# Performance work log

Hardware: AMD Instinct MI355X
Metric: run time of the kernel (lower is better)

The kernel has to match this reference:

```python
import jax, jax.numpy as jnp
import numpy as np

B, N, E = 8, 10000, 320000
HIST, PRED = 24, 12
IN_DIM, GNN_OUT, HID = 17, 13, 64


def setup_inputs() -> dict:
    key = jax.random.key(0)
    ks = jax.random.split(key, 16)
    rn = lambda k, s, sc=0.1: jax.random.normal(k, s, jnp.float32) * sc
    return {
        "t2m_hist": jax.random.normal(ks[0], (B, HIST, N, 1), jnp.float32),
        "feature": jax.random.normal(ks[1], (B, HIST + PRED, N, IN_DIM - 1), jnp.float32),
        "edge_index": jax.random.randint(ks[2], (2, E), 0, N),
        "edge_attr": jax.random.normal(ks[3], (E, 1), jnp.float32),
        "edge_w1": rn(ks[4], (2 * IN_DIM + 1, 32)),
        "edge_b1": rn(ks[5], (32,)),
        "edge_w2": rn(ks[6], (32, 30)),
        "edge_b2": rn(ks[7], (30,)),
        "node_w": rn(ks[8], (30, GNN_OUT)),
        "node_b": rn(ks[9], (GNN_OUT,)),
        "gru_wih": rn(ks[10], (3 * HID, IN_DIM + GNN_OUT)),
        "gru_whh": rn(ks[11], (3 * HID, HID)),
        "gru_bih": rn(ks[12], (3 * HID,)),
        "gru_bhh": rn(ks[13], (3 * HID,)),
        "fc_out_w": rn(ks[14], (HID, 1)),
        "fc_out_b": rn(ks[15], (1,)),
    }


def reference(t2m_hist, feature, edge_index, edge_attr,
              edge_w1, edge_b1, edge_w2, edge_b2, node_w, node_b,
              gru_wih, gru_whh, gru_bih, gru_bhh, fc_out_w, fc_out_b):
    src, tgt = edge_index[0], edge_index[1]
    # edge_attr normalized with unbiased std (torch default)
    ea_norm = (edge_attr - edge_attr.mean(0)) / edge_attr.std(0, ddof=1)  # [E,1]

    def graph_gnn(x):  # x: [B,N,IN_DIM]
        ns = x[:, src]                                  # [B,E,IN_DIM] gather
        nt = x[:, tgt]                                  # [B,E,IN_DIM] gather
        ea = jnp.broadcast_to(ea_norm[None], (B, E, 1))
        h = jnp.concatenate([ns, nt, ea], axis=-1)      # [B,E,2*IN_DIM+1]
        h = jax.nn.sigmoid(h @ edge_w1 + edge_b1)
        h = jax.nn.sigmoid(h @ edge_w2 + edge_b2)       # [B,E,30]
        agg = jnp.zeros((B, N, 30), h.dtype)
        agg = agg.at[:, tgt].add(h)                     # scatter_add to targets
        agg = agg.at[:, src].add(-h)                    # scatter_add(-) to sources
        return jax.nn.sigmoid(agg @ node_w + node_b)    # [B,N,GNN_OUT]

    def gru(xin, h):  # xin: [M,30], h: [M,HID]  (PyTorch GRUCell math)
        gi = xin @ gru_wih.T + gru_bih
        gh = h @ gru_whh.T + gru_bhh
        i_r, i_z, i_n = jnp.split(gi, 3, axis=-1)
        h_r, h_z, h_n = jnp.split(gh, 3, axis=-1)
        r = jax.nn.sigmoid(i_r + h_r)
        z = jax.nn.sigmoid(i_z + h_z)
        n = jnp.tanh(i_n + r * h_n)
        return (1.0 - z) * n + z * h

    feat_future = jnp.moveaxis(feature[:, HIST:HIST + PRED], 1, 0)  # [PRED,B,N,16]
    h0 = jnp.zeros((B * N, HID), jnp.float32)
    xn0 = t2m_hist[:, -1]  # [B,N,1]

    def step(carry, feat_t):
        hn, xn = carry
        x = jnp.concatenate([xn, feat_t], axis=-1)      # [B,N,IN_DIM]
        g = graph_gnn(x)                                # [B,N,GNN_OUT]
        xin = jnp.concatenate([g, x], axis=-1).reshape(B * N, IN_DIM + GNN_OUT)
        hn = gru(xin, hn)
        xn = hn.reshape(B, N, HID) @ fc_out_w + fc_out_b  # [B,N,1]
        return (hn, xn), xn

    _, preds = jax.lax.scan(step, (h0, xn0), feat_future)  # [PRED,B,N,1]
    return jnp.moveaxis(preds, 0, 1)                        # [B,PRED,N,1]
```

## Files before the change

### kernel.cpp

```cpp
#include <hip/hip_runtime.h>
#include <hip/hip_fp16.h>
#include <hip/hip_bf16.h>

#define Bb 8
#define Nn 10000
#define Ee 320000
#define HIST 24
#define PRED 12
#define BN (Bb * Nn)

__device__ __forceinline__ float sigm(float x) { return 1.0f / (1.0f + __expf(-x)); }
__device__ __forceinline__ float tanh_fast(float x) { return 1.0f - 2.0f / (__expf(2.0f * x) + 1.0f); }

__device__ __forceinline__ void load16f(const float* p, float* o) {
  const float4* q = reinterpret_cast<const float4*>(p);
  float4 a = q[0], b = q[1], c = q[2], d = q[3];
  o[0] = a.x; o[1] = a.y; o[2]  = a.z; o[3]  = a.w;
  o[4] = b.x; o[5] = b.y; o[6]  = b.z; o[7]  = b.w;
  o[8] = c.x; o[9] = c.y; o[10] = c.z; o[11] = c.w;
  o[12] = d.x; o[13] = d.y; o[14] = d.z; o[15] = d.w;
}

__device__ __forceinline__ void edge_mlp(const float* __restrict__ in,
                                         const float* __restrict__ W,
                                         float* __restrict__ h2) {
  const float* w1 = W;
  const float* b1 = W + 1120;
  const float* w2 = W + 1152;
  const float* b2 = W + 2112;
  float h1[32];
#pragma unroll
  for (int j = 0; j < 32; j++) h1[j] = b1[j];
#pragma unroll
  for (int k = 0; k < 35; k++) {
    float v = in[k];
#pragma unroll
    for (int j = 0; j < 32; j++) h1[j] = fmaf(v, w1[k * 32 + j], h1[j]);
  }
#pragma unroll
  for (int j = 0; j < 32; j++) h1[j] = sigm(h1[j]);
#pragma unroll
  for (int j = 0; j < 30; j++) h2[j] = b2[j];
#pragma unroll
  for (int k = 0; k < 32; k++) {
    float v = h1[k];
#pragma unroll
    for (int j = 0; j < 30; j++) h2[j] = fmaf(v, w2[k * 30 + j], h2[j]);
  }
#pragma unroll
  for (int j = 0; j < 30; j++) h2[j] = sigm(h2[j]);
}

__device__ __forceinline__ void gru_out(const float* __restrict__ agg,
                                        const float* __restrict__ W,
                                        const float* __restrict__ featp,
                                        float xn_old,
                                        float* __restrict__ xn_new_slot,
                                        float* __restrict__ hp,
                                        float* __restrict__ out_slot) {
  const float* nw  = W + 2142;
  const float* nb  = W + 2532;
  const float* wih = W + 2545;
  const float* whh = W + 8305;
  const float* bih = W + 20593;
  const float* bhh = W + 20785;
  const float* fw  = W + 20977;
  const float* fcb = W + 21041;
  float xin[30];
#pragma unroll
  for (int j = 0; j < 13; j++) {
    float a = nb[j];
#pragma unroll
    for (int k = 0; k < 30; k++) a = fmaf(agg[k], nw[k * 13 + j], a);
    xin[j] = sigm(a);
  }
  xin[13] = xn_old;
  load16f(featp, xin + 14);
  float h[64];
#pragma unroll
  for (int j = 0; j < 64; j++) h[j] = hp[j];
  float xnew = fcb[0];
  for (int j = 0; j < 64; j++) {
    float ir = bih[j], iz = bih[64 + j], inn = bih[128 + j];
    const float* wr = wih + j * 30;
    const float* wz = wih + (64 + j) * 30;
    const float* wn = wih + (128 + j) * 30;
#pragma unroll
    for (int k = 0; k < 30; k++) {
      ir  = fmaf(xin[k], wr[k], ir);
      iz  = fmaf(xin[k], wz[k], iz);
      inn = fmaf(xin[k], wn[k], inn);
    }
    float hr = bhh[j], hz = bhh[64 + j], hn_ = bhh[128 + j];
    const float* vr = whh + j * 64;
    const float* vz = whh + (64 + j) * 64;
    const float* vn = whh + (128 + j) * 64;
#pragma unroll
    for (int k = 0; k < 64; k++) {
      hr  = fmaf(h[k], vr[k], hr);
      hz  = fmaf(h[k], vz[k], hz);
      hn_ = fmaf(h[k], vn[k], hn_);
    }
    float rg = sigm(ir + hr);
    float zg = sigm(iz + hz);
    float ng = tanh_fast(inn + rg * hn_);
    float hnew = (1.f - zg) * ng + zg * h[j];
    hp[j] = hnew;
    xnew = fmaf(hnew, fw[j], xnew);
  }
  *xn_new_slot = xnew;
  *out_slot = xnew;
}


__global__ void k_stats(const float* __restrict__ ea, float* __restrict__ stats) {
  __shared__ float s1[256], s2[256];
  int tid = threadIdx.x;
  int i = blockIdx.x * 256 + tid;
  float v = 0.f;
  if (i < Ee) v = ea[i];
  s1[tid] = v;
  s2[tid] = v * v;
  __syncthreads();
  for (int o = 128; o > 0; o >>= 1) {
    if (tid < o) { s1[tid] += s1[tid + o]; s2[tid] += s2[tid + o]; }
    __syncthreads();
  }
  if (tid == 0) { atomicAdd(&stats[0], s1[0]); atomicAdd(&stats[1], s2[0]); }
}

__global__ void k_finalize_stats(float* stats) {
  float sum = stats[0], sumsq = stats[1];
  float mean = sum / (float)Ee;
  float var = (sumsq - sum * mean) / (float)(Ee - 1);
  stats[2] = mean;
  stats[3] = rsqrtf(var);
}

__global__ void k_hist(const int* __restrict__ eidx, int* __restrict__ deg_t, int* __restrict__ deg_s) {
  int e = blockIdx.x * 256 + threadIdx.x;
  if (e >= Ee) return;
  atomicAdd(&deg_s[eidx[e]], 1);
  atomicAdd(&deg_t[eidx[Ee + e]], 1);
}

__global__ void k_scan(const int* __restrict__ deg_t, int* __restrict__ off_t,
                       const int* __restrict__ deg_s, int* __restrict__ off_s) {
  const int* deg = (blockIdx.x == 0) ? deg_t : deg_s;
  int* off = (blockIdx.x == 0) ? off_t : off_s;
  __shared__ int s[1024];
  __shared__ int carry;
  int tid = threadIdx.x;
  if (tid == 0) carry = 0;
  __syncthreads();
  for (int base = 0; base < Nn; base += 1024) {
    int v = (base + tid < Nn) ? deg[base + tid] : 0;
    s[tid] = v;
    int val = v;
    __syncthreads();
    for (int o = 1; o < 1024; o <<= 1) {
      int tv = (tid >= o) ? s[tid - o] : 0;
      __syncthreads();
      val += tv;
      s[tid] = val;
      __syncthreads();
    }
    if (base + tid < Nn) off[base + tid] = carry + (val - v);
    __syncthreads();
    if (tid == 1023) carry += val;
    __syncthreads();
  }
  if (tid == 0) off[Nn] = carry;
}

__global__ void k_fill(const int* __restrict__ eidx,
                       const int* __restrict__ off_t, const int* __restrict__ off_s,
                       int* __restrict__ cur_t, int* __restrict__ cur_s,
                       int* __restrict__ list_t, int* __restrict__ list_s) {
  int e = blockIdx.x * 256 + threadIdx.x;
  if (e >= Ee) return;
  int s = eidx[e], t = eidx[Ee + e];
  int ps = off_s[s] + atomicAdd(&cur_s[s], 1);
  list_s[ps] = e;
  int pt = off_t[t] + atomicAdd(&cur_t[t], 1);
  list_t[pt] = e;
}

__global__ void k_convert(const float* w1, const float* b1, const float* w2, const float* b2,
                          const float* nw, const float* nb, const float* wih, const float* whh,
                          const float* bih, const float* bhh, const float* fw, const float* fb,
                          float* __restrict__ dst) {
  int i = blockIdx.x * 256 + threadIdx.x;
  const int c1 = 1120, c2 = 1152, c3 = 2112, c4 = 2142, c5 = 2532, c6 = 2545,
            c7 = 8305, c8 = 20593, c9 = 20785, c10 = 20977, c11 = 21041, c12 = 21042;
  if (i >= c12) return;
  const float* p;
  int base;
  if (i < c1)       { p = w1;  base = 0;  }
  else if (i < c2)  { p = b1;  base = c1; }
  else if (i < c3)  { p = w2;  base = c2; }
  else if (i < c4)  { p = b2;  base = c3; }
  else if (i < c5)  { p = nw;  base = c4; }
  else if (i < c6)  { p = nb;  base = c5; }
  else if (i < c7)  { p = wih; base = c6; }
  else if (i < c8)  { p = whh; base = c7; }
  else if (i < c9)  { p = bih; base = c8; }
  else if (i < c10) { p = bhh; base = c9; }
  else if (i < c11) { p = fw;  base = c10; }
  else              { p = fb;  base = c11; }
  dst[i] = p[i - base];
}

__global__ void k_xn0(const float* __restrict__ t2m, float* __restrict__ xn) {
  int i = blockIdx.x * 256 + threadIdx.x;
  if (i >= BN) return;
  int b = i / Nn, n = i % Nn;
  xn[i] = t2m[((size_t)b * HIST + (HIST - 1)) * Nn + n];
}


__global__ __launch_bounds__(256) void k_pre_edge(
    const float* __restrict__ feat, const float* __restrict__ xn,
    const float* __restrict__ W, float* __restrict__ as_, float* __restrict__ at_, int t) {
  int idx = blockIdx.x * 256 + threadIdx.x;
  if (idx >= BN) return;
  int b = idx / Nn, n = idx % Nn;
  const float* w1 = W;
  const float* b1 = W + 1120;
  float f[16];
  const float* fbp = feat + ((size_t)(b * (HIST + PRED) + HIST + t)) * Nn * 16 + (size_t)n * 16;
  load16f(fbp, f);
  float x = xn[idx];
  float as[32], at[32];
#pragma unroll
  for (int j = 0; j < 32; j++) {
    as[j] = fmaf(x, w1[j], b1[j]);
    at[j] = x * w1[17 * 32 + j];
  }
#pragma unroll
  for (int k = 0; k < 16; k++) {
    float v = f[k];
#pragma unroll
    for (int j = 0; j < 32; j++) {
      as[j] = fmaf(v, w1[(1 + k) * 32 + j], as[j]);
      at[j] = fmaf(v, w1[(18 + k) * 32 + j], at[j]);
    }
  }
  float4* ap = (float4*)(as_ + (size_t)idx * 32);
  float4* bp = (float4*)(at_ + (size_t)idx * 32);
#pragma unroll
  for (int q = 0; q < 8; q++) {
    ap[q] = make_float4(as[4 * q], as[4 * q + 1], as[4 * q + 2], as[4 * q + 3]);
    bp[q] = make_float4(at[4 * q], at[4 * q + 1], at[4 * q + 2], at[4 * q + 3]);
  }
}

__global__ __launch_bounds__(256) void k_edge2(
    const int* __restrict__ eidx, const float* __restrict__ ea,
    const float* __restrict__ as_, const float* __restrict__ at_,
    const float* __restrict__ W, const float* __restrict__ stats,
    __half* __restrict__ h2out) {
  int e = blockIdx.x * 256 + threadIdx.x;
  int b = blockIdx.y;
  if (e >= Ee) return;
  float mean = stats[2], istd = stats[3];
  int s = eidx[e], tg = eidx[Ee + e];
  float ean = (ea[e] - mean) * istd;
  const float* w1e = W + 34 * 32;
  const float* w2 = W + 1152;
  const float* b2 = W + 2112;
  const float4* ap = (const float4*)(as_ + ((size_t)(b * Nn + s)) * 32);
  const float4* bp = (const float4*)(at_ + ((size_t)(b * Nn + tg)) * 32);
  float h1[32];
#pragma unroll
  for (int q = 0; q < 8; q++) {
    float4 av = ap[q], bv = bp[q];
    h1[4 * q]     = av.x + bv.x;
    h1[4 * q + 1] = av.y + bv.y;
    h1[4 * q + 2] = av.z + bv.z;
    h1[4 * q + 3] = av.w + bv.w;
  }
#pragma unroll
  for (int j = 0; j < 32; j++) h1[j] = sigm(fmaf(ean, w1e[j], h1[j]));
  float h2[30];
#pragma unroll
  for (int j = 0; j < 30; j++) h2[j] = b2[j];
#pragma unroll
  for (int k = 0; k < 32; k++) {
    float v = h1[k];
#pragma unroll
    for (int j = 0; j < 30; j++) h2[j] = fmaf(v, w2[k * 30 + j], h2[j]);
  }
  __half2* o = (__half2*)(h2out + ((size_t)b * Ee + e) * 30);
#pragma unroll
  for (int i = 0; i < 15; i++) o[i] = __floats2half2_rn(sigm(h2[2 * i]), sigm(h2[2 * i + 1]));
}

__global__ __launch_bounds__(256) void k_edge(
    const int* __restrict__ eidx, const float* __restrict__ ea,
    const float* __restrict__ feat, const float* __restrict__ xn,
    const float* __restrict__ W, const float* __restrict__ stats,
    __half* __restrict__ h2out, int t) {
  int e = blockIdx.x * 256 + threadIdx.x;
  int b = blockIdx.y;
  if (e >= Ee) return;
  float mean = stats[2], istd = stats[3];
  int s = eidx[e], tg = eidx[Ee + e];
  float in[35];
  in[0]  = xn[b * Nn + s];
  in[17] = xn[b * Nn + tg];
  in[34] = (ea[e] - mean) * istd;
  const float* fb = feat + ((size_t)(b * (HIST + PRED) + HIST + t)) * Nn * 16;
  load16f(fb + (size_t)s * 16, in + 1);
  load16f(fb + (size_t)tg * 16, in + 18);
  float h2[30];
  edge_mlp(in, W, h2);
  __half2* o = (__half2*)(h2out + ((size_t)b * Ee + e) * 30);
#pragma unroll
  for (int i = 0; i < 15; i++) o[i] = __floats2half2_rn(h2[2 * i], h2[2 * i + 1]);
}

__global__ __launch_bounds__(256) void k_gather(
    const int* __restrict__ off_t, const int* __restrict__ list_t,
    const int* __restrict__ off_s, const int* __restrict__ list_s,
    const __half* __restrict__ h2, float* __restrict__ agg) {
  int tid = threadIdx.x;
  int c = tid & 31;
  int idx = blockIdx.x * 8 + (tid >> 5);
  if (idx >= BN || c >= 30) return;
  int b = idx / Nn, n = idx % Nn;
  const __half* base = h2 + (size_t)b * Ee * 30;
  float a = 0.f;
  int p0 = off_t[n], p1 = off_t[n + 1];
  int p = p0;
  for (; p + 4 <= p1; p += 4) {
    int e0 = list_t[p], e1 = list_t[p + 1], e2 = list_t[p + 2], e3 = list_t[p + 3];
    float v0 = __half2float(base[(size_t)e0 * 30 + c]);
    float v1 = __half2float(base[(size_t)e1 * 30 + c]);
    float v2 = __half2float(base[(size_t)e2 * 30 + c]);
    float v3 = __half2float(base[(size_t)e3 * 30 + c]);
    a += (v0 + v1) + (v2 + v3);
  }
  for (; p < p1; p++) a += __half2float(base[(size_t)list_t[p] * 30 + c]);
  p0 = off_s[n]; p1 = off_s[n + 1];
  p = p0;
  for (; p + 4 <= p1; p += 4) {
    int e0 = list_s[p], e1 = list_s[p + 1], e2 = list_s[p + 2], e3 = list_s[p + 3];
    float v0 = __half2float(base[(size_t)e0 * 30 + c]);
    float v1 = __half2float(base[(size_t)e1 * 30 + c]);
    float v2 = __half2float(base[(size_t)e2 * 30 + c]);
    float v3 = __half2float(base[(size_t)e3 * 30 + c]);
    a -= (v0 + v1) + (v2 + v3);
  }
  for (; p < p1; p++) a -= __half2float(base[(size_t)list_s[p] * 30 + c]);
  agg[(size_t)idx * 30 + c] = a;
}

#define HS_STRIDE 68

__global__ __launch_bounds__(256, 4) void k_gru4(
    const float* __restrict__ agg_all, const float* __restrict__ W,
    const float* __restrict__ feat, const float* __restrict__ xn_cur,
    float* __restrict__ xn_nxt, float* __restrict__ hbuf,
    float* __restrict__ out, int t) {
  __shared__ float hs[64 * HS_STRIDE];
  __shared__ float sx[4][64];

  const int tid = threadIdx.x;
  const int lane = tid & 63;
  const int wave = (int)__builtin_amdgcn_readfirstlane(tid >> 6);
  const int node = blockIdx.x * 64 + lane;
  const int b = node / Nn, n = node % Nn;

  const float* nw  = W + 2142;
  const float* nb  = W + 2532;
  const float* wih = W + 2545;
  const float* whh = W + 8305;
  const float* bih = W + 20593;
  const float* bhh = W + 20785;
  const float* fw  = W + 20977;
  const float* fcb = W + 21041;

  float* hp = hbuf + node;
  {
    const int k0 = wave * 16;
#pragma unroll
    for (int kk = 0; kk < 16; kk++) {
      int k = k0 + kk;
      hs[lane * HS_STRIDE + k] = hp[(size_t)k * BN];
    }
  }

  float xin[30];
  {
    float agg[30];
    const float* ap = agg_all + (size_t)node * 30;
#pragma unroll
    for (int i = 0; i < 30; i++) agg[i] = ap[i];
#pragma unroll
    for (int j = 0; j < 13; j++) {
      float a = nb[j];
#pragma unroll
      for (int k = 0; k < 30; k++) a = fmaf(agg[k], nw[k * 13 + j], a);
      xin[j] = sigm(a);
    }
  }
  xin[13] = xn_cur[node];
  const float* fbp = feat + ((size_t)(b * (HIST + PRED) + HIST + t)) * Nn * 16 + (size_t)n * 16;
  load16f(fbp, xin + 14);

  __syncthreads();

  const int j0 = wave * 16;
  const float* hrow = hs + lane * HS_STRIDE;
  float xpart = 0.f;
  for (int jj = 0; jj < 16; jj++) {
    const int j = j0 + jj;
    float ir = bih[j], iz = bih[64 + j], inn = bih[128 + j];
    const float* wr = wih + j * 30;
    const float* wz = wih + (64 + j) * 30;
    const float* wn = wih + (128 + j) * 30;
#pragma unroll
    for (int k = 0; k < 30; k++) {
      ir  = fmaf(xin[k], wr[k], ir);
      iz  = fmaf(xin[k], wz[k], iz);
      inn = fmaf(xin[k], wn[k], inn);
    }
    float hr = bhh[j], hz = bhh[64 + j], hn_ = bhh[128 + j];
    const float* vr = whh + j * 64;
    const float* vz = whh + (64 + j) * 64;
    const float* vn = whh + (128 + j) * 64;
#pragma unroll
    for (int k4 = 0; k4 < 16; k4++) {
      float4 h4 = *reinterpret_cast<const float4*>(hrow + k4 * 4);
      hr  = fmaf(h4.x, vr[4 * k4],     hr);
      hz  = fmaf(h4.x, vz[4 * k4],     hz);
      hn_ = fmaf(h4.x, vn[4 * k4],     hn_);
      hr  = fmaf(h4.y, vr[4 * k4 + 1], hr);
      hz  = fmaf(h4.y, vz[4 * k4 + 1], hz);
      hn_ = fmaf(h4.y, vn[4 * k4 + 1], hn_);
      hr  = fmaf(h4.z, vr[4 * k4 + 2], hr);
      hz  = fmaf(h4.z, vz[4 * k4 + 2], hz);
      hn_ = fmaf(h4.z, vn[4 * k4 + 2], hn_);
      hr  = fmaf(h4.w, vr[4 * k4 + 3], hr);
      hz  = fmaf(h4.w, vz[4 * k4 + 3], hz);
      hn_ = fmaf(h4.w, vn[4 * k4 + 3], hn_);
    }
    float holdj = hrow[j];
    float rg = sigm(ir + hr);
    float zg = sigm(iz + hz);
    float ng = tanh_fast(inn + rg * hn_);
    float hnew = (1.f - zg) * ng + zg * holdj;
    hp[(size_t)j * BN] = hnew;
    xpart = fmaf(hnew, fw[j], xpart);
  }

  sx[wave][lane] = xpart;
  __syncthreads();
  if (wave == 0) {
    float xnew = fcb[0] + ((sx[0][lane] + sx[1][lane]) + (sx[2][lane] + sx[3][lane]));
    xn_nxt[node] = xnew;
    out[((size_t)b * PRED + t) * Nn + n] = xnew;
  }
}


__global__ __launch_bounds__(64) void k_node_g(
    const int* __restrict__ off_t, const int* __restrict__ list_t,
    const int* __restrict__ off_s, const int* __restrict__ list_s,
    const __half* __restrict__ h2, const float* __restrict__ W,
    const float* __restrict__ feat, const float* __restrict__ xn_cur,
    float* __restrict__ xn_nxt,
    float* __restrict__ hbuf, float* __restrict__ out, int t) {
  int n = blockIdx.x * 64 + threadIdx.x;
  int b = blockIdx.y;
  if (n >= Nn) return;
  float agg[30];
#pragma unroll
  for (int i = 0; i < 30; i++) agg[i] = 0.f;
  int p0 = off_t[n], p1 = off_t[n + 1];
  for (int p = p0; p < p1; p++) {
    int e = list_t[p];
    const __half2* r = (const __half2*)(h2 + ((size_t)b * Ee + e) * 30);
#pragma unroll
    for (int i = 0; i < 15; i++) {
      __half2 v = r[i];
      agg[2 * i]     += __low2float(v);
      agg[2 * i + 1] += __high2float(v);
    }
  }
  p0 = off_s[n]; p1 = off_s[n + 1];
  for (int p = p0; p < p1; p++) {
    int e = list_s[p];
    const __half2* r = (const __half2*)(h2 + ((size_t)b * Ee + e) * 30);
#pragma unroll
    for (int i = 0; i < 15; i++) {
      __half2 v = r[i];
      agg[2 * i]     -= __low2float(v);
      agg[2 * i + 1] -= __high2float(v);
    }
  }
  const float* fbp = feat + ((size_t)(b * (HIST + PRED) + HIST + t)) * Nn * 16 + (size_t)n * 16;
  gru_out(agg, W, fbp, xn_cur[b * Nn + n], &xn_nxt[b * Nn + n],
          hbuf + ((size_t)b * Nn + n) * 64, &out[((size_t)b * PRED + t) * Nn + n]);
}


__global__ __launch_bounds__(128) void k_node_rc(
    const int* __restrict__ eidx, const float* __restrict__ ea,
    const int* __restrict__ off_t, const int* __restrict__ list_t,
    const int* __restrict__ off_s, const int* __restrict__ list_s,
    const float* __restrict__ W, const float* __restrict__ stats,
    const float* __restrict__ feat, const float* __restrict__ xn_cur,
    float* __restrict__ xn_nxt,
    float* __restrict__ hbuf, float* __restrict__ out, int t) {
  int idx = blockIdx.x * 128 + threadIdx.x;
  if (idx >= BN) return;
  int b = idx / Nn, n = idx % Nn;
  float mean = stats[2], istd = stats[3];
  const float* fslice = feat + ((size_t)(b * (HIST + PRED) + HIST + t)) * Nn * 16;
  float xo = xn_cur[b * Nn + n];
  float fo[16];
  load16f(fslice + (size_t)n * 16, fo);
  float agg[30];
#pragma unroll
  for (int i = 0; i < 30; i++) agg[i] = 0.f;
  float in[35], h2e[30];
  int p0 = off_t[n], p1 = off_t[n + 1];
  for (int p = p0; p < p1; p++) {
    int e = list_t[p];
    int s = eidx[e];
    in[0] = xn_cur[b * Nn + s];
    load16f(fslice + (size_t)s * 16, in + 1);
    in[17] = xo;
#pragma unroll
    for (int i = 0; i < 16; i++) in[18 + i] = fo[i];
    in[34] = (ea[e] - mean) * istd;
    edge_mlp(in, W, h2e);
#pragma unroll
    for (int i = 0; i < 30; i++) agg[i] += h2e[i];
  }
  p0 = off_s[n]; p1 = off_s[n + 1];
  for (int p = p0; p < p1; p++) {
    int e = list_s[p];
    int tg = eidx[Ee + e];
    in[0] = xo;
#pragma unroll
    for (int i = 0; i < 16; i++) in[1 + i] = fo[i];
    in[17] = xn_cur[b * Nn + tg];
    load16f(fslice + (size_t)tg * 16, in + 18);
    in[34] = (ea[e] - mean) * istd;
    edge_mlp(in, W, h2e);
#pragma unroll
    for (int i = 0; i < 30; i++) agg[i] -= h2e[i];
  }
  gru_out(agg, W, fslice + (size_t)n * 16, xo, &xn_nxt[b * Nn + n],
          hbuf + ((size_t)b * Nn + n) * 64, &out[((size_t)b * PRED + t) * Nn + n]);
}


extern "C" void kernel_launch(void* const* d_in, const int* in_sizes, int n_in,
                              void* d_out, int out_size, void* d_ws, size_t ws_size,
                              hipStream_t stream) {
  const float* t2m  = (const float*)d_in[0];
  const float* feat = (const float*)d_in[1];
  const int*   eidx = (const int*)d_in[2];
  const float* ea   = (const float*)d_in[3];
  const float* w1   = (const float*)d_in[4];
  const float* b1   = (const float*)d_in[5];
  const float* w2   = (const float*)d_in[6];
  const float* b2   = (const float*)d_in[7];
  const float* nw   = (const float*)d_in[8];
  const float* nb   = (const float*)d_in[9];
  const float* wih  = (const float*)d_in[10];
  const float* whh  = (const float*)d_in[11];
  const float* bih  = (const float*)d_in[12];
  const float* bhh  = (const float*)d_in[13];
  const float* fw   = (const float*)d_in[14];
  const float* fb   = (const float*)d_in[15];
  float* out = (float*)d_out;

  float* ws = (float*)d_ws;
  float* stats = ws;
  int* deg_t = (int*)(ws + 4);
  int* deg_s = deg_t + Nn;
  int* cur_t = deg_s + Nn;
  int* cur_s = cur_t + Nn;
  float* hbuf = (float*)(cur_s + Nn);
  int* off_t = (int*)(hbuf + (size_t)BN * 64);
  int* off_s = off_t + (Nn + 1);
  int* list_t = off_s + (Nn + 1);
  int* list_s = list_t + Ee;
  float* Wf = (float*)(list_s + Ee);
  float* xnA = Wf + 21056;
  float* xnB = xnA + BN;
  float* base_end = xnB + BN;
  size_t base_bytes = (size_t)((char*)base_end - (char*)d_ws);
  base_bytes = (base_bytes + 15) & ~(size_t)15;
  __half* h2buf = (__half*)((char*)d_ws + base_bytes);
  size_t mid_bytes = base_bytes + (size_t)Bb * Ee * 30 * sizeof(__half);
  mid_bytes = (mid_bytes + 15) & ~(size_t)15;
  float* aggbuf = (float*)((char*)d_ws + mid_bytes);
  size_t big_bytes = mid_bytes + (size_t)BN * 30 * sizeof(float);
  big_bytes = (big_bytes + 15) & ~(size_t)15;
  float* asbuf = (float*)((char*)d_ws + big_bytes);
  float* atbuf = asbuf + (size_t)BN * 32;
  size_t need_big2 = big_bytes + 2 * (size_t)BN * 32 * sizeof(float);
  bool big2 = ws_size >= need_big2;
  bool big  = ws_size >= big_bytes;
  bool mid  = ws_size >= mid_bytes;

  size_t zero_bytes = (size_t)(4 + 4 * Nn + (size_t)BN * 64) * 4;
  hipMemsetAsync(d_ws, 0, zero_bytes, stream);

  k_stats<<<dim3((Ee + 255) / 256), 256, 0, stream>>>(ea, stats);
  k_finalize_stats<<<1, 1, 0, stream>>>(stats);
  k_hist<<<dim3((Ee + 255) / 256), 256, 0, stream>>>(eidx, deg_t, deg_s);
  k_scan<<<2, 1024, 0, stream>>>(deg_t, off_t, deg_s, off_s);
  k_fill<<<dim3((Ee + 255) / 256), 256, 0, stream>>>(eidx, off_t, off_s, cur_t, cur_s, list_t, list_s);
  k_convert<<<dim3((21042 + 255) / 256), 256, 0, stream>>>(w1, b1, w2, b2, nw, nb, wih, whh, bih, bhh, fw, fb, Wf);
  k_xn0<<<dim3((BN + 255) / 256), 256, 0, stream>>>(t2m, xnA);

  for (int t = 0; t < PRED; t++) {
    float* xc  = (t & 1) ? xnB : xnA;
    float* xnx = (t & 1) ? xnA : xnB;
    if (big2) {
      k_pre_edge<<<dim3((BN + 255) / 256), 256, 0, stream>>>(feat, xc, Wf, asbuf, atbuf, t);
      k_edge2<<<dim3((Ee + 255) / 256, Bb), 256, 0, stream>>>(eidx, ea, asbuf, atbuf, Wf, stats, h2buf);
      k_gather<<<dim3((BN + 7) / 8), 256, 0, stream>>>(off_t, list_t, off_s, list_s, h2buf, aggbuf);
      k_gru4<<<dim3(BN / 64), 256, 0, stream>>>(aggbuf, Wf, feat, xc, xnx, hbuf, out, t);
    } else if (big) {
      k_edge<<<dim3((Ee + 255) / 256, Bb), 256, 0, stream>>>(eidx, ea, feat, xc, Wf, stats, h2buf, t);
      k_gather<<<dim3((BN + 7) / 8), 256, 0, stream>>>(off_t, list_t, off_s, list_s, h2buf, aggbuf);
      k_gru4<<<dim3(BN / 64), 256, 0, stream>>>(aggbuf, Wf, feat, xc, xnx, hbuf, out, t);
    } else if (mid) {
      k_edge<<<dim3((Ee + 255) / 256, Bb), 256, 0, stream>>>(eidx, ea, feat, xc, Wf, stats, h2buf, t);
      k_node_g<<<dim3((Nn + 63) / 64, Bb), 64, 0, stream>>>(off_t, list_t, off_s, list_s, h2buf, Wf, feat, xc, xnx, hbuf, out, t);
    } else {
      k_node_rc<<<dim3((BN + 127) / 128), 128, 0, stream>>>(eidx, ea, off_t, list_t, off_s, list_s, Wf, stats, feat, xc, xnx, hbuf, out, t);
    }
  }
}
```

Before: 5.640 ms.

## Share node-projection work across waves via LDS in GRU kernel

Previously every wave in the GRU block recomputed the full 30x13 node projection for its 64 nodes and loaded agg and features redundantly. Now agg rows are staged into LDS with coalesced float4 loads, the projection is split across all 256 threads (4 outputs per thread), and feature and xn loads are assigned to single waves, with results shared through an LDS xin buffer. This removes the 4x redundant projection compute and the redundant global loads. In exchange it adds extra LDS use (about 15KB more) and an extra barrier, which may lower occupancy. The part==3 path also writes only one of its four outputs, which is correct since there are 13 outputs.

New measurement: 6.866 ms. +21.7%, slower.

```diff
diff --git a/kernel.cpp b/kernel.cpp
--- a/kernel.cpp
+++ b/kernel.cpp
@@ -357,6 +357,7 @@
 }
 
 #define HS_STRIDE 68
+#define XIN_STRIDE 31
 
 __global__ __launch_bounds__(256, 4) void k_gru4(
     const float* __restrict__ agg_all, const float* __restrict__ W,
@@ -364,12 +365,15 @@
     float* __restrict__ xn_nxt, float* __restrict__ hbuf,
     float* __restrict__ out, int t) {
   __shared__ float hs[64 * HS_STRIDE];
+  __shared__ float xs[64 * XIN_STRIDE];
+  __shared__ float agg_lds[1920];
   __shared__ float sx[4][64];
 
   const int tid = threadIdx.x;
   const int lane = tid & 63;
   const int wave = (int)__builtin_amdgcn_readfirstlane(tid >> 6);
-  const int node = blockIdx.x * 64 + lane;
+  const int blk0 = blockIdx.x * 64;
+  const int node = blk0 + lane;
   const int b = node / Nn, n = node % Nn;
 
   const float* nw  = W + 2142;
@@ -382,6 +386,17 @@
   const float* fcb = W + 21041;
 
   float* hp = hbuf + node;
+
+  {
+    const float4* src = (const float4*)(agg_all + (size_t)blk0 * 30);
+    float4 v0 = src[tid];
+    ((float4*)agg_lds)[tid] = v0;
+    if (tid < 224) {
+      float4 v1 = src[256 + tid];
+      ((float4*)agg_lds)[256 + tid] = v1;
+    }
+  }
+
   {
     const int k0 = wave * 16;
 #pragma unroll
@@ -391,25 +406,47 @@
     }
   }
 
+  if (wave == 2) {
+    float f[16];
+    const float* fbp = feat + ((size_t)(b * (HIST + PRED) + HIST + t)) * Nn * 16 + (size_t)n * 16;
+    load16f(fbp, f);
+#pragma unroll
+    for (int i = 0; i < 16; i++) xs[lane * XIN_STRIDE + 14 + i] = f[i];
+  } else if (wave == 1) {
+    xs[lane * XIN_STRIDE + 13] = xn_cur[node];
+  }
+
+  __syncthreads();
+
+  {
+    const int node_m = tid >> 2;
+    const int part = tid & 3;
+    const float* ar = agg_lds + node_m * 30;
+    float a0 = nb[4 * part + 0], a1 = nb[4 * part + 1],
+          a2 = nb[4 * part + 2], a3 = nb[4 * part + 3];
+#pragma unroll
+    for (int k = 0; k < 30; k++) {
+      float v = ar[k];
+      const float* wrow = nw + k * 13 + 4 * part;
+      a0 = fmaf(v, wrow[0], a0);
+      a1 = fmaf(v, wrow[1], a1);
+      a2 = fmaf(v, wrow[2], a2);
+      a3 = fmaf(v, wrow[3], a3);
+    }
+    float* xrow = xs + node_m * XIN_STRIDE + 4 * part;
+    if (part < 3) {
+      xrow[0] = sigm(a0); xrow[1] = sigm(a1);
+      xrow[2] = sigm(a2); xrow[3] = sigm(a3);
+    } else {
+      xrow[0] = sigm(a0);
+    }
+  }
+
+  __syncthreads();
+
   float xin[30];
-  {
-    float agg[30];
-    const float* ap = agg_all + (size_t)node * 30;
-#pragma unroll
-    for (int i = 0; i < 30; i++) agg[i] = ap[i];
-#pragma unroll
-    for (int j = 0; j < 13; j++) {
-      float a = nb[j];
-#pragma unroll
-      for (int k = 0; k < 30; k++) a = fmaf(agg[k], nw[k * 13 + j], a);
-      xin[j] = sigm(a);
-    }
-  }
-  xin[13] = xn_cur[node];
-  const float* fbp = feat + ((size_t)(b * (HIST + PRED) + HIST + t)) * Nn * 16 + (size_t)n * 16;
-  load16f(fbp, xin + 14);
-
-  __syncthreads();
+#pragma unroll
+  for (int k = 0; k < 30; k++) xin[k] = xs[lane * XIN_STRIDE + k];
 
   const int j0 = wave * 16;
   const float* hrow = hs + lane * HS_STRIDE;
```

## Fuse edge MLP into CSR-based per-node gather, dropping the fp16 edge buffer

Applied to the files above, without the earlier changes.

Replaces the per-edge MLP kernel and the separate gather kernel with one node-centric kernel. Each node walks its incoming and outgoing CSR edge lists, computes the edge MLP in registers and accumulates the sums directly, with two thread halves handling the target and source roles and combining them through shared memory. This removes the write and re-read of the large [B,E,30] half-precision edge buffer. In exchange, every edge MLP is computed twice (once from each endpoint), and thread loop lengths follow node degree, so warps can diverge.

Result: slower. 14.88 ms (+163.8%).

```diff
diff --git a/kernel.cpp b/kernel.cpp
--- a/kernel.cpp
+++ b/kernel.cpp
@@ -255,45 +255,90 @@
   }
 }
 
-__global__ __launch_bounds__(256) void k_edge2(
+__global__ __launch_bounds__(256, 2) void k_egather(
     const int* __restrict__ eidx, const float* __restrict__ ea,
+    const int* __restrict__ off_t, const int* __restrict__ list_t,
+    const int* __restrict__ off_s, const int* __restrict__ list_s,
     const float* __restrict__ as_, const float* __restrict__ at_,
     const float* __restrict__ W, const float* __restrict__ stats,
-    __half* __restrict__ h2out) {
-  int e = blockIdx.x * 256 + threadIdx.x;
-  int b = blockIdx.y;
-  if (e >= Ee) return;
-  float mean = stats[2], istd = stats[3];
-  int s = eidx[e], tg = eidx[Ee + e];
-  float ean = (ea[e] - mean) * istd;
-  const float* w1e = W + 34 * 32;
-  const float* w2 = W + 1152;
-  const float* b2 = W + 2112;
-  const float4* ap = (const float4*)(as_ + ((size_t)(b * Nn + s)) * 32);
-  const float4* bp = (const float4*)(at_ + ((size_t)(b * Nn + tg)) * 32);
-  float h1[32];
-#pragma unroll
-  for (int q = 0; q < 8; q++) {
-    float4 av = ap[q], bv = bp[q];
-    h1[4 * q]     = av.x + bv.x;
-    h1[4 * q + 1] = av.y + bv.y;
-    h1[4 * q + 2] = av.z + bv.z;
-    h1[4 * q + 3] = av.w + bv.w;
-  }
-#pragma unroll
-  for (int j = 0; j < 32; j++) h1[j] = sigm(fmaf(ean, w1e[j], h1[j]));
-  float h2[30];
-#pragma unroll
-  for (int j = 0; j < 30; j++) h2[j] = b2[j];
-#pragma unroll
-  for (int k = 0; k < 32; k++) {
-    float v = h1[k];
-#pragma unroll
-    for (int j = 0; j < 30; j++) h2[j] = fmaf(v, w2[k * 30 + j], h2[j]);
-  }
-  __half2* o = (__half2*)(h2out + ((size_t)b * Ee + e) * 30);
-#pragma unroll
-  for (int i = 0; i < 15; i++) o[i] = __floats2half2_rn(sigm(h2[2 * i]), sigm(h2[2 * i + 1]));
+    float* __restrict__ agg_out) {
+  __shared__ float sagg[128 * 30];
+  const int tid = threadIdx.x;
+  const int m = tid & 127;
+  const int role = tid >> 7;
+  const int blk0 = blockIdx.x * 128;
+  const int node = blk0 + m;
+  const int b = node / Nn, n = node % Nn;
+  const float mean = stats[2], istd = stats[3];
+  const float* w1e = W + 1088;
+  const float* w2  = W + 1152;
+  const float* b2  = W + 2112;
+
+  float own[32];
+  {
+    const float4* q = (const float4*)((role ? as_ : at_) + (size_t)(b * Nn + n) * 32);
+#pragma unroll
+    for (int i = 0; i < 8; i++) {
+      float4 v = q[i];
+      own[4 * i] = v.x; own[4 * i + 1] = v.y; own[4 * i + 2] = v.z; own[4 * i + 3] = v.w;
+    }
+  }
+  const int* off = role ? off_s : off_t;
+  const int* lst = role ? list_s : list_t;
+  const int* nbx = role ? (eidx + Ee) : eidx;
+  const float* nbase = role ? at_ : as_;
+
+  float agg[30];
+#pragma unroll
+  for (int i = 0; i < 30; i++) agg[i] = 0.f;
+
+  const int p1 = off[n + 1];
+  for (int p = off[n]; p < p1; p++) {
+    int e = lst[p];
+    int nb = nbx[e];
+    float ean = (ea[e] - mean) * istd;
+    const float4* nq = (const float4*)(nbase + (size_t)(b * Nn + nb) * 32);
+    float h1[32];
+#pragma unroll
+    for (int i = 0; i < 8; i++) {
+      float4 v = nq[i];
+      h1[4 * i]     = sigm(fmaf(ean, w1e[4 * i],     own[4 * i]     + v.x));
+      h1[4 * i + 1] = sigm(fmaf(ean, w1e[4 * i + 1], own[4 * i + 1] + v.y));
+      h1[4 * i + 2] = sigm(fmaf(ean, w1e[4 * i + 2], own[4 * i + 2] + v.z));
+      h1[4 * i + 3] = sigm(fmaf(ean, w1e[4 * i + 3], own[4 * i + 3] + v.w));
+    }
+    float h2[30];
+#pragma unroll
+    for (int j = 0; j < 30; j++) h2[j] = b2[j];
+#pragma unroll
+    for (int k = 0; k < 32; k++) {
+      float v = h1[k];
+#pragma unroll
+      for (int j = 0; j < 30; j++) h2[j] = fmaf(v, w2[k * 30 + j], h2[j]);
+    }
+#pragma unroll
+    for (int j = 0; j < 30; j++) agg[j] += sigm(h2[j]);
+  }
+
+  if (role == 1) {
+#pragma unroll
+    for (int j = 0; j < 30; j++) sagg[m * 30 + j] = agg[j];
+  }
+  __syncthreads();
+  if (role == 0) {
+#pragma unroll
+    for (int j = 0; j < 30; j++) sagg[m * 30 + j] = agg[j] - sagg[m * 30 + j];
+  }
+  __syncthreads();
+  {
+    float4* dst = (float4*)(agg_out + (size_t)blk0 * 30);
+    const float4* src4 = (const float4*)sagg;
+#pragma unroll
+    for (int r = 0; r < 4; r++) {
+      int i = r * 256 + tid;
+      if (i < 960) dst[i] = src4[i];
+    }
+  }
 }
 
 __global__ __launch_bounds__(256) void k_edge(
@@ -626,8 +671,8 @@
     float* xnx = (t & 1) ? xnA : xnB;
     if (big2) {
       k_pre_edge<<<dim3((BN + 255) / 256), 256, 0, stream>>>(feat, xc, Wf, asbuf, atbuf, t);
-      k_edge2<<<dim3((Ee + 255) / 256, Bb), 256, 0, stream>>>(eidx, ea, asbuf, atbuf, Wf, stats, h2buf);
-      k_gather<<<dim3((BN + 7) / 8), 256, 0, stream>>>(off_t, list_t, off_s, list_s, h2buf, aggbuf);
+      k_egather<<<dim3(BN / 128), 256, 0, stream>>>(eidx, ea, off_t, list_t, off_s, list_s,
+                                                    asbuf, atbuf, Wf, stats, aggbuf);
       k_gru4<<<dim3(BN / 64), 256, 0, stream>>>(aggbuf, Wf, feat, xc, xnx, hbuf, out, t);
     } else if (big) {
       k_edge<<<dim3((Ee + 255) / 256, Bb), 256, 0, stream>>>(eidx, ea, feat, xc, Wf, stats, h2buf, t);
```

## Interleave edge outputs across batch and gather all batches per node in one wave

Applied to the files above, without the earlier changes.

The edge kernel now writes its fp16 outputs edge-major, with all 8 batches' 30 channels stored contiguously (240 halves per edge). A new gather kernel assigns one wave per node and reads each incident edge's full 480-byte row with coalesced half2 loads, covering every batch at once. Edge-list and offset reads are shared across batches, and per-edge memory access becomes one contiguous segment instead of eight scattered ones. In exchange, the edge kernel's stores are now strided per batch (60 bytes out of a 480-byte row per block row), and 8 of the 64 lanes sit idle on the second load.

Measured after the change: 5.410 ms. 1.04x faster.

```diff
diff --git a/kernel.cpp b/kernel.cpp
--- a/kernel.cpp
+++ b/kernel.cpp
@@ -259,7 +259,7 @@
     const int* __restrict__ eidx, const float* __restrict__ ea,
     const float* __restrict__ as_, const float* __restrict__ at_,
     const float* __restrict__ W, const float* __restrict__ stats,
-    __half* __restrict__ h2out) {
+    __half* __restrict__ h2p) {
   int e = blockIdx.x * 256 + threadIdx.x;
   int b = blockIdx.y;
   if (e >= Ee) return;
@@ -291,9 +291,78 @@
 #pragma unroll
     for (int j = 0; j < 30; j++) h2[j] = fmaf(v, w2[k * 30 + j], h2[j]);
   }
-  __half2* o = (__half2*)(h2out + ((size_t)b * Ee + e) * 30);
+  __half2* o = (__half2*)(h2p + (size_t)e * 240 + b * 30);
 #pragma unroll
   for (int i = 0; i < 15; i++) o[i] = __floats2half2_rn(sigm(h2[2 * i]), sigm(h2[2 * i + 1]));
+}
+
+__global__ __launch_bounds__(256) void k_gather8(
+    const int* __restrict__ off_t, const int* __restrict__ list_t,
+    const int* __restrict__ off_s, const int* __restrict__ list_s,
+    const __half* __restrict__ h2p, float* __restrict__ agg) {
+  const int lane = threadIdx.x & 63;
+  const int wave = threadIdx.x >> 6;
+  const int n = blockIdx.x * 4 + wave;
+  const bool hasP1 = (lane < 56);
+
+  float a0x = 0.f, a0y = 0.f, a1x = 0.f, a1y = 0.f;
+
+  int p0 = off_t[n], p1 = off_t[n + 1];
+  int p = p0;
+  for (; p + 2 <= p1; p += 2) {
+    int e0 = list_t[p], e1 = list_t[p + 1];
+    const __half2* r0 = (const __half2*)(h2p + (size_t)e0 * 240);
+    const __half2* r1 = (const __half2*)(h2p + (size_t)e1 * 240);
+    __half2 u0 = r0[lane];
+    __half2 v0 = r1[lane];
+    __half2 u1 = hasP1 ? r0[lane + 64] : __half2{};
+    __half2 v1 = hasP1 ? r1[lane + 64] : __half2{};
+    a0x += __low2float(u0) + __low2float(v0);
+    a0y += __high2float(u0) + __high2float(v0);
+    a1x += __low2float(u1) + __low2float(v1);
+    a1y += __high2float(u1) + __high2float(v1);
+  }
+  for (; p < p1; p++) {
+    int e0 = list_t[p];
+    const __half2* r0 = (const __half2*)(h2p + (size_t)e0 * 240);
+    __half2 u0 = r0[lane];
+    __half2 u1 = hasP1 ? r0[lane + 64] : __half2{};
+    a0x += __low2float(u0); a0y += __high2float(u0);
+    a1x += __low2float(u1); a1y += __high2float(u1);
+  }
+  p0 = off_s[n]; p1 = off_s[n + 1];
+  p = p0;
+  for (; p + 2 <= p1; p += 2) {
+    int e0 = list_s[p], e1 = list_s[p + 1];
+    const __half2* r0 = (const __half2*)(h2p + (size_t)e0 * 240);
+    const __half2* r1 = (const __half2*)(h2p + (size_t)e1 * 240);
+    __half2 u0 = r0[lane];
+    __half2 v0 = r1[lane];
+    __half2 u1 = hasP1 ? r0[lane + 64] : __half2{};
+    __half2 v1 = hasP1 ? r1[lane + 64] : __half2{};
+    a0x -= __low2float(u0) + __low2float(v0);
+    a0y -= __high2float(u0) + __high2float(v0);
+    a1x -= __low2float(u1) + __low2float(v1);
+    a1y -= __high2float(u1) + __high2float(v1);
+  }
+  for (; p < p1; p++) {
+    int e0 = list_s[p];
+    const __half2* r0 = (const __half2*)(h2p + (size_t)e0 * 240);
+    __half2 u0 = r0[lane];
+    __half2 u1 = hasP1 ? r0[lane + 64] : __half2{};
+    a0x -= __low2float(u0); a0y -= __high2float(u0);
+    a1x -= __low2float(u1); a1y -= __high2float(u1);
+  }
+
+  {
+    int b0 = lane / 15, c0 = (lane % 15) * 2;
+    *(float2*)(agg + ((size_t)b0 * Nn + n) * 30 + c0) = make_float2(a0x, a0y);
+    if (hasP1) {
+      int P1i = lane + 64;
+      int b1 = P1i / 15, c1 = (P1i % 15) * 2;
+      *(float2*)(agg + ((size_t)b1 * Nn + n) * 30 + c1) = make_float2(a1x, a1y);
+    }
+  }
 }
 
 __global__ __launch_bounds__(256) void k_edge(
@@ -627,7 +696,7 @@
     if (big2) {
       k_pre_edge<<<dim3((BN + 255) / 256), 256, 0, stream>>>(feat, xc, Wf, asbuf, atbuf, t);
       k_edge2<<<dim3((Ee + 255) / 256, Bb), 256, 0, stream>>>(eidx, ea, asbuf, atbuf, Wf, stats, h2buf);
-      k_gather<<<dim3((BN + 7) / 8), 256, 0, stream>>>(off_t, list_t, off_s, list_s, h2buf, aggbuf);
+      k_gather8<<<dim3(Nn / 4), 256, 0, stream>>>(off_t, list_t, off_s, list_s, h2buf, aggbuf);
       k_gru4<<<dim3(BN / 64), 256, 0, stream>>>(aggbuf, Wf, feat, xc, xnx, hbuf, out, t);
     } else if (big) {
       k_edge<<<dim3((Ee + 255) / 256, Bb), 256, 0, stream>>>(eidx, ea, feat, xc, Wf, stats, h2buf, t);
```
